# Performance work log

Hardware: AMD Instinct MI355X
Metric: run time of the kernel (lower is better)

The kernel has to match this reference:

```python
import jax, jax.numpy as jnp
import numpy as np

BETA_MEM = 0.9
BETA_INH = 0.6
THRESHOLD = 1.0  # snn.Leaky default


def setup_inputs() -> dict:
    key = jax.random.key(0)
    k1, = jax.random.split(key, 1)
    T, B = 1024, 16384
    spike_seq = (jax.random.uniform(k1, (T, B, 2)) < 0.05).astype(jnp.float32)
    w_exc = jnp.array([[0.7, 1.0]], dtype=jnp.float32)  # fc_exc.weight, [1, 2]
    w_inh = jnp.array(-1.0, dtype=jnp.float32)          # scalar inhibitory weight
    return {"spike_seq": spike_seq, "w_exc": w_exc, "w_inh": w_inh}


@jax.custom_vjp
def spike_fn(x):
    # Heaviside spike with ATan surrogate gradient (snntorch default, alpha=2)
    return (x > 0).astype(x.dtype)

def _spike_fwd(x):
    return spike_fn(x), x

def _spike_bwd(x, g):
    return (g / (1.0 + (jnp.pi * x) ** 2),)

spike_fn.defvjp(_spike_fwd, _spike_bwd)


def reference(spike_seq, w_exc, w_inh):
    T, B, _ = spike_seq.shape
    mem0 = jnp.zeros((B, 1), dtype=spike_seq.dtype)
    inh0 = jnp.zeros((B, 1), dtype=spike_seq.dtype)

    def step(carry, x_t):
        mem, inh = carry
        cur_exc = x_t @ w_exc.T                      # [B, 1]
        fm1 = x_t[:, 0:1]                            # [B, 1]
        inh = BETA_INH * inh + fm1
        cur = cur_exc + w_inh * inh
        # snn.Leaky: reset (subtract) computed from previous mem, detached
        reset = jax.lax.stop_gradient((mem - THRESHOLD > 0).astype(mem.dtype))
        mem = BETA_MEM * mem + cur - reset * THRESHOLD
        spk = spike_fn(mem - THRESHOLD)
        return (mem, inh), (spk, mem)

    _, (spk_rec, mem_rec) = jax.lax.scan(step, (mem0, inh0), spike_seq)
    return spk_rec, mem_rec  # each [T, B, 1]
```

## Files before the change

### kernel.cpp

```cpp
#include <hip/hip_runtime.h>

#define T_LEN 1024
#define B_N   16384
#define NSEG  8
#define SEGT  (T_LEN / NSEG)
#define GN    256
#define CW_WORDS (B_N * (T_LEN / 16))

__global__ __launch_bounds__(256) void k1_compress(
    const float* __restrict__ x, unsigned int* __restrict__ cw) {
  const int tid = blockIdx.x * 256 + threadIdx.x;
  const int pn  = tid & (B_N / 2 - 1);
  const int j   = tid >> 13;
  const float4* xp4 = (const float4*)x;
  unsigned int wA = 0, wB = 0;
#pragma unroll
  for (int k = 0; k < 16; ++k) {
    const float4 v = xp4[(size_t)(16 * j + k) * (B_N / 2) + pn];
    wA |= (v.x != 0.0f ? 1u : 0u) << (2 * k);
    wA |= (v.y != 0.0f ? 1u : 0u) << (2 * k + 1);
    wB |= (v.z != 0.0f ? 1u : 0u) << (2 * k);
    wB |= (v.w != 0.0f ? 1u : 0u) << (2 * k + 1);
  }
  ((uint2*)cw)[(size_t)j * (B_N / 2) + pn] = make_uint2(wA, wB);
}

__global__ __launch_bounds__(64, 1) void k2a_checkpoint(
    const unsigned int* __restrict__ cw,
    const float* __restrict__ w_exc, const float* __restrict__ w_inh,
    float2* __restrict__ chk) {
#pragma clang fp contract(off)
  const int n = blockIdx.x * 64 + threadIdx.x;
  const float w0 = w_exc[0], w1 = w_exc[1], wi = w_inh[0];
  float mem = 0.0f, inh = 0.0f;
  unsigned int A = cw[n];
  unsigned int Bw = cw[(size_t)1 * B_N + n];
  unsigned int C = cw[(size_t)2 * B_N + n];
  unsigned int D = cw[(size_t)3 * B_N + n];

#define STEP16(W)                                                   \
  _Pragma("unroll") for (int k = 0; k < 16; ++k) {                  \
    const float x0 = (float)(((W) >> (2 * k)) & 1u);                \
    const float x1 = (float)(((W) >> (2 * k + 1)) & 1u);            \
    const float cur_exc = x0 * w0 + x1 * w1;   \
    inh = 0.6f * inh + x0;                                          \
    const float cur = cur_exc + wi * inh;          \
    const float reset = (mem > 1.0f) ? 1.0f : 0.0f;                 \
    mem = 0.9f * mem + cur - reset;           \
  }

  for (int j = 0; j < 56; j += 4) {
    unsigned int nA = 0, nB = 0, nC = 0, nD = 0;
    if (j + 4 < 56) {
      nA = cw[(size_t)(j + 4) * B_N + n];
      nB = cw[(size_t)(j + 5) * B_N + n];
      nC = cw[(size_t)(j + 6) * B_N + n];
      nD = cw[(size_t)(j + 7) * B_N + n];
    }
    __builtin_amdgcn_sched_barrier(0);
    STEP16(A) STEP16(Bw) STEP16(C) STEP16(D)
    if (((j + 4) & 7) == 0)
      chk[(size_t)(((j + 4) >> 3) - 1) * B_N + n] = make_float2(mem, inh);
    A = nA; Bw = nB; C = nC; D = nD;
  }
#undef STEP16
}

__global__ __launch_bounds__(256, 2) void FMFMNeuronInhib_34033320854098_kernel(
    const unsigned int* __restrict__ cw, const float2* __restrict__ chk,
    const float* __restrict__ w_exc, const float* __restrict__ w_inh,
    float* __restrict__ out) {
#pragma clang fp contract(off)
  const int seg = blockIdx.x >> 6;
  const int g   = blockIdx.x & 63;
  const int n   = g * GN + threadIdx.x;

  float* __restrict__ spk_out = out;
  float* __restrict__ mem_out = out + (size_t)T_LEN * B_N;

  const float w0 = w_exc[0], w1 = w_exc[1], wi = w_inh[0];
  float mem = 0.0f, inh = 0.0f;
  if (seg > 0) {
    const float2 c = chk[(size_t)(seg - 1) * B_N + n];
    mem = c.x;
    inh = c.y;
  }
  unsigned int w[8];
#pragma unroll
  for (int j = 0; j < 8; ++j) w[j] = cw[(size_t)(seg * 8 + j) * B_N + n];

#pragma unroll
  for (int j = 0; j < 8; ++j) {
#pragma unroll
    for (int k = 0; k < 16; ++k) {
      const int t = seg * SEGT + j * 16 + k;
      const float x0 = (float)((w[j] >> (2 * k)) & 1u);
      const float x1 = (float)((w[j] >> (2 * k + 1)) & 1u);
      const float cur_exc = x0 * w0 + x1 * w1;
      inh = 0.6f * inh + x0;
      const float cur = cur_exc + wi * inh;
      const float reset = (mem > 1.0f) ? 1.0f : 0.0f;
      mem = 0.9f * mem + cur - reset;
      const float spk = (mem > 1.0f) ? 1.0f : 0.0f;
      const size_t idx = (size_t)t * B_N + n;
      spk_out[idx] = spk;
      mem_out[idx] = mem;
    }
    __builtin_amdgcn_s_barrier();
  }
}

extern "C" void kernel_launch(void* const* d_in, const int* in_sizes, int n_in,
                              void* d_out, int out_size, void* d_ws, size_t ws_size,
                              hipStream_t stream) {
  const float* x     = (const float*)d_in[0];
  const float* w_exc = (const float*)d_in[1];
  const float* w_inh = (const float*)d_in[2];
  float* out = (float*)d_out;
  unsigned int* cw = (unsigned int*)d_ws;
  float2* chk = (float2*)((char*)d_ws + (size_t)CW_WORDS * 4);

  hipLaunchKernelGGL(k1_compress, dim3(CW_WORDS / 2 / 256), dim3(256), 0,
                     stream, x, cw);
  hipLaunchKernelGGL(k2a_checkpoint, dim3(B_N / 64), dim3(64), 0, stream,
                     cw, w_exc, w_inh, chk);
  hipLaunchKernelGGL(FMFMNeuronInhib_34033320854098_kernel,
                     dim3(NSEG * (B_N / GN)), dim3(GN), 0, stream,
                     cw, chk, w_exc, w_inh, out);
}
```

Before: 270.3 us.

## Checkpoint every 8 steps and vectorize output writes across many short segments

The checkpoint pass now stores state every 8 (or 16) timesteps over the full sequence instead of 8 coarse segments. The output kernel is reorganized so each thread handles 16 neurons over only 4 timesteps. It replays from the nearest checkpoint and emits float4 stores for spike and membrane outputs. This aims to cut the serial per-thread recurrence length in the output kernel and widen stores. The cost is more checkpoint writes and more sequential work in the single-wave-per-block checkpoint kernel, plus a workspace-size-dependent path choice.

Measured after the change: 284.1 us. 1.05x slower.

```diff
diff --git a/kernel.cpp b/kernel.cpp
--- a/kernel.cpp
+++ b/kernel.cpp
@@ -1,10 +1,8 @@
 #include <hip/hip_runtime.h>
+#include <stdint.h>
 
 #define T_LEN 1024
 #define B_N   16384
-#define NSEG  8
-#define SEGT  (T_LEN / NSEG)
-#define GN    256
 #define CW_WORDS (B_N * (T_LEN / 16))
 
 __global__ __launch_bounds__(256) void k1_compress(
@@ -28,7 +26,7 @@
 __global__ __launch_bounds__(64, 1) void k2a_checkpoint(
     const unsigned int* __restrict__ cw,
     const float* __restrict__ w_exc, const float* __restrict__ w_inh,
-    float2* __restrict__ chk) {
+    float2* __restrict__ chk, int ivl8) {
 #pragma clang fp contract(off)
   const int n = blockIdx.x * 64 + threadIdx.x;
   const float w0 = w_exc[0], w1 = w_exc[1], wi = w_inh[0];
@@ -38,76 +36,116 @@
   unsigned int C = cw[(size_t)2 * B_N + n];
   unsigned int D = cw[(size_t)3 * B_N + n];
 
-#define STEP16(W)                                                   \
-  _Pragma("unroll") for (int k = 0; k < 16; ++k) {                  \
-    const float x0 = (float)(((W) >> (2 * k)) & 1u);                \
-    const float x1 = (float)(((W) >> (2 * k + 1)) & 1u);            \
-    const float cur_exc = x0 * w0 + x1 * w1;   \
-    inh = 0.6f * inh + x0;                                          \
-    const float cur = cur_exc + wi * inh;          \
-    const float reset = (mem > 1.0f) ? 1.0f : 0.0f;                 \
-    mem = 0.9f * mem + cur - reset;           \
+#define STEP8(W, KB)                                                 \
+  _Pragma("unroll") for (int k = (KB); k < (KB) + 8; ++k) {          \
+    const float x0 = (float)(((W) >> (2 * k)) & 1u);                 \
+    const float x1 = (float)(((W) >> (2 * k + 1)) & 1u);             \
+    const float cur_exc = x0 * w0 + x1 * w1;    \
+    inh = 0.6f * inh + x0;                                           \
+    const float cur = cur_exc + wi * inh;           \
+    const float reset = (mem > 1.0f) ? 1.0f : 0.0f;                  \
+    mem = 0.9f * mem + cur - reset;            \
+  }
+#define WORD(W, JW)                                                  \
+  {                                                                  \
+    STEP8(W, 0)                                                      \
+    if (ivl8) chk[(size_t)(2 * (JW)) * B_N + n] = make_float2(mem, inh); \
+    STEP8(W, 8)                                                      \
+    if ((JW) <= 62)                                                  \
+      chk[(size_t)(ivl8 ? 2 * (JW) + 1 : (JW)) * B_N + n] =          \
+          make_float2(mem, inh);                                     \
   }
 
-  for (int j = 0; j < 56; j += 4) {
+  for (int j = 0; j < 64; j += 4) {
     unsigned int nA = 0, nB = 0, nC = 0, nD = 0;
-    if (j + 4 < 56) {
+    if (j + 4 < 64) {
       nA = cw[(size_t)(j + 4) * B_N + n];
       nB = cw[(size_t)(j + 5) * B_N + n];
       nC = cw[(size_t)(j + 6) * B_N + n];
       nD = cw[(size_t)(j + 7) * B_N + n];
     }
     __builtin_amdgcn_sched_barrier(0);
-    STEP16(A) STEP16(Bw) STEP16(C) STEP16(D)
-    if (((j + 4) & 7) == 0)
-      chk[(size_t)(((j + 4) >> 3) - 1) * B_N + n] = make_float2(mem, inh);
+    WORD(A, j) WORD(Bw, j + 1) WORD(C, j + 2) WORD(D, j + 3)
     A = nA; Bw = nB; C = nC; D = nD;
   }
-#undef STEP16
+#undef WORD
+#undef STEP8
 }
 
-__global__ __launch_bounds__(256, 2) void FMFMNeuronInhib_34033320854098_kernel(
+__global__ __launch_bounds__(512, 2) void FMFMNeuronInhib_34033320854098_kernel(
     const unsigned int* __restrict__ cw, const float2* __restrict__ chk,
     const float* __restrict__ w_exc, const float* __restrict__ w_inh,
-    float* __restrict__ out) {
+    float* __restrict__ out, int ivl) {
 #pragma clang fp contract(off)
-  const int seg = blockIdx.x >> 6;
-  const int g   = blockIdx.x & 63;
-  const int n   = g * GN + threadIdx.x;
+  const int tid = threadIdx.x;
+  const int bx  = blockIdx.x;
+  const int h   = bx & 1;
+  const int r   = bx >> 1;
+  const int ivl8 = (ivl == 8);
+  const int q = ivl8 ? (r & 1) : (r & 3);
+  const int s = ivl8 ? (r >> 1) : (r >> 2);
+  const int tseg = s * ivl;
+  const int tw   = tseg + 4 * q;
+  const int j0   = tw >> 4;
+  const int kd0  = tseg & 15;
+  const int kw0  = tw & 15;
 
+  const float w0 = w_exc[0], w1 = w_exc[1], wi = w_inh[0];
   float* __restrict__ spk_out = out;
   float* __restrict__ mem_out = out + (size_t)T_LEN * B_N;
 
-  const float w0 = w_exc[0], w1 = w_exc[1], wi = w_inh[0];
-  float mem = 0.0f, inh = 0.0f;
-  if (seg > 0) {
-    const float2 c = chk[(size_t)(seg - 1) * B_N + n];
-    mem = c.x;
-    inh = c.y;
+  uint4 wv[4];
+  float mem[4][4], inh[4][4];
+#pragma unroll
+  for (int c = 0; c < 4; ++c) {
+    const int nc = h * 8192 + c * 2048 + 4 * tid;
+    wv[c] = *(const uint4*)&cw[(size_t)j0 * B_N + nc];
+    if (s > 0) {
+      const float4* cp = (const float4*)&chk[(size_t)(s - 1) * B_N + nc];
+      const float4 a = cp[0], b = cp[1];
+      mem[c][0] = a.x; inh[c][0] = a.y; mem[c][1] = a.z; inh[c][1] = a.w;
+      mem[c][2] = b.x; inh[c][2] = b.y; mem[c][3] = b.z; inh[c][3] = b.w;
+    } else {
+#pragma unroll
+      for (int m = 0; m < 4; ++m) { mem[c][m] = 0.0f; inh[c][m] = 0.0f; }
+    }
   }
-  unsigned int w[8];
+
+#define NSTEP(c, m, W)                                              \
+  {                                                                 \
+    const float x0 = (float)(((W) >> (2 * k)) & 1u);                \
+    const float x1 = (float)(((W) >> (2 * k + 1)) & 1u);            \
+    const float cur_exc = x0 * w0 + x1 * w1;                        \
+    inh[c][m] = 0.6f * inh[c][m] + x0;                              \
+    const float cur = cur_exc + wi * inh[c][m];                     \
+    const float reset = (mem[c][m] > 1.0f) ? 1.0f : 0.0f;           \
+    mem[c][m] = 0.9f * mem[c][m] + cur - reset;                     \
+  }
+
+  for (int k = kd0; k < kw0; ++k) {
 #pragma unroll
-  for (int j = 0; j < 8; ++j) w[j] = cw[(size_t)(seg * 8 + j) * B_N + n];
-
+    for (int c = 0; c < 4; ++c) {
+      NSTEP(c, 0, wv[c].x) NSTEP(c, 1, wv[c].y)
+      NSTEP(c, 2, wv[c].z) NSTEP(c, 3, wv[c].w)
+    }
+  }
+  for (int k = kw0; k < kw0 + 4; ++k) {
+    const int t = (j0 << 4) + k;
 #pragma unroll
-  for (int j = 0; j < 8; ++j) {
-#pragma unroll
-    for (int k = 0; k < 16; ++k) {
-      const int t = seg * SEGT + j * 16 + k;
-      const float x0 = (float)((w[j] >> (2 * k)) & 1u);
-      const float x1 = (float)((w[j] >> (2 * k + 1)) & 1u);
-      const float cur_exc = x0 * w0 + x1 * w1;
-      inh = 0.6f * inh + x0;
-      const float cur = cur_exc + wi * inh;
-      const float reset = (mem > 1.0f) ? 1.0f : 0.0f;
-      mem = 0.9f * mem + cur - reset;
-      const float spk = (mem > 1.0f) ? 1.0f : 0.0f;
-      const size_t idx = (size_t)t * B_N + n;
-      spk_out[idx] = spk;
-      mem_out[idx] = mem;
+    for (int c = 0; c < 4; ++c) {
+      NSTEP(c, 0, wv[c].x) NSTEP(c, 1, wv[c].y)
+      NSTEP(c, 2, wv[c].z) NSTEP(c, 3, wv[c].w)
+      float4 sv, mv;
+      sv.x = (mem[c][0] > 1.0f) ? 1.0f : 0.0f; mv.x = mem[c][0];
+      sv.y = (mem[c][1] > 1.0f) ? 1.0f : 0.0f; mv.y = mem[c][1];
+      sv.z = (mem[c][2] > 1.0f) ? 1.0f : 0.0f; mv.z = mem[c][2];
+      sv.w = (mem[c][3] > 1.0f) ? 1.0f : 0.0f; mv.w = mem[c][3];
+      const size_t base = (size_t)t * B_N + h * 8192 + c * 2048 + 4 * tid;
+      *(float4*)&spk_out[base] = sv;
+      *(float4*)&mem_out[base] = mv;
     }
-    __builtin_amdgcn_s_barrier();
   }
+#undef NSTEP
 }
 
 extern "C" void kernel_launch(void* const* d_in, const int* in_sizes, int n_in,
@@ -118,13 +156,15 @@
   const float* w_inh = (const float*)d_in[2];
   float* out = (float*)d_out;
   unsigned int* cw = (unsigned int*)d_ws;
-  float2* chk = (float2*)((char*)d_ws + (size_t)CW_WORDS * 4);
+  float2* chk = (float2*)((char*)d_ws + ((size_t)CW_WORDS * 4));
+
+  const size_t need8 = (size_t)CW_WORDS * 4 + (size_t)127 * B_N * 8;
+  const int ivl = (ws_size == 0 || ws_size >= need8) ? 8 : 16;
 
   hipLaunchKernelGGL(k1_compress, dim3(CW_WORDS / 2 / 256), dim3(256), 0,
                      stream, x, cw);
   hipLaunchKernelGGL(k2a_checkpoint, dim3(B_N / 64), dim3(64), 0, stream,
-                     cw, w_exc, w_inh, chk);
-  hipLaunchKernelGGL(FMFMNeuronInhib_34033320854098_kernel,
-                     dim3(NSEG * (B_N / GN)), dim3(GN), 0, stream,
-                     cw, chk, w_exc, w_inh, out);
+                     cw, w_exc, w_inh, chk, ivl == 8 ? 1 : 0);
+  hipLaunchKernelGGL(FMFMNeuronInhib_34033320854098_kernel, dim3(512),
+                     dim3(512), 0, stream, cw, chk, w_exc, w_inh, out, ivl);
 }
```
